# Kernel tuning notes

Measured on AMD Instinct MI355X. Metric: run time of the kernel, lower is better.

## Reference

```python
import jax, jax.numpy as jnp
import numpy as np

B, C, H, W = 256, 200, 32, 32


def setup_inputs() -> dict:
    key = jax.random.key(0)
    x = jax.random.normal(key, (B, C, H, W), dtype=jnp.float32)
    # exact init of the torch nn.Parameter: log(3.2 / c^2) * ones(1,1)
    temperature = jnp.log(3.2 / (C * C)) * jnp.ones((1, 1), dtype=jnp.float32)
    return {"x": x, "temperature": temperature}


def reference(x, temperature):
    b, c, h, w = x.shape
    xf = x.reshape(b, c, h * w)                     # (B, c, hw)
    # Gram matrix x @ x^T  -> (B, c, c)
    G = jnp.einsum('bcm,bdm->bcd', xf, xf)
    # diagonal of G = squared norms per band  -> (B, c)
    d = jnp.einsum('bcm,bcm->bc', xf, xf)
    # I_M @ (G*I) puts d_j in every row; (G*I) @ I_M puts d_i in every column
    dcov = d[:, None, :] + d[:, :, None] - 2.0 * G  # (B, c, c)
    dcov = jnp.maximum(dcov, 0.0)
    dcov = jnp.sqrt(jnp.exp(temperature)[0, 0] * dcov + 1e-5)
    # double centering: dcov@I_M/c = row means, I_M@dcov/c = col means,
    # I_M@dcov@I_M/c^2 = global mean (per batch element)
    row_mean = jnp.mean(dcov, axis=2, keepdims=True)
    col_mean = jnp.mean(dcov, axis=1, keepdims=True)
    tot_mean = jnp.mean(dcov, axis=(1, 2), keepdims=True)
    return -(dcov - row_mean - col_mean + tot_mean)
```

## Files before the change

### kernel.cpp

```cpp
#include <hip/hip_runtime.h>
#include <hip/hip_bf16.h>

typedef __bf16 bf16x8 __attribute__((ext_vector_type(8)));
typedef float  f32x4  __attribute__((ext_vector_type(4)));

#define C_DIM   200
#define HW_DIM  1024
#define NT      13
#define PADC    208
#define BK      64
#define NKC     16
#define ROWB    128
#define TILEB   (PADC*ROWB)
#define SLAB    (PADC*HW_DIM)

#define GLD16(gp, lp) __builtin_amdgcn_global_load_lds(                      \
    (const __attribute__((address_space(1))) unsigned int*)(gp),             \
    (__attribute__((address_space(3))) unsigned int*)(lp), 16, 0, 0)

__device__ __forceinline__ bf16x8 pack8(float4 a, float4 b){
  bf16x8 v;
  v[0]=(__bf16)a.x; v[1]=(__bf16)a.y; v[2]=(__bf16)a.z; v[3]=(__bf16)a.w;
  v[4]=(__bf16)b.x; v[5]=(__bf16)b.y; v[6]=(__bf16)b.z; v[7]=(__bf16)b.w;
  return v;
}

__global__ __launch_bounds__(832, 4)
void spectral_corr_kernel(const float* __restrict__ x,
                          const float* __restrict__ temp,
                          float* __restrict__ out,
                          __hip_bfloat16* __restrict__ ws)
{
  __shared__ __align__(16) char sA[2][TILEB];
  __shared__ float d_lds[PADC];
  __shared__ float rs_lds[PADC];

  const int tid = threadIdx.x;
  const int b   = blockIdx.x;
  const int w   = tid >> 6;
  const int l   = tid & 63;
  const int g   = l >> 4;
  const int c   = l & 15;

  const float*    xb = x  + (size_t)b * (C_DIM * HW_DIM);
  __hip_bfloat16* wb = ws + (size_t)b * SLAB;

  const int r_a  = tid >> 3,        c8_a = tid & 7;
  const int s_b  = tid + 832;
  const int r_b  = s_b >> 3,        c8_b = s_b & 7;
  const bool vb  = (s_b < 1600);

  const int si = l >> 3;
  const int sc = (l & 7) ^ si;
  const int i0 = 2*w, i1 = 2*w + 1;
  const __hip_bfloat16* gs0 = wb + (size_t)(8*i0 + si)*HW_DIM + sc*8;
  const __hip_bfloat16* gs1 = wb + (size_t)(8*i1 + si)*HW_DIM + sc*8;

  f32x4 acc[NT];
  #pragma unroll
  for (int j=0;j<NT;++j) acc[j] = (f32x4){0.f,0.f,0.f,0.f};

  #pragma unroll
  for (int cc = 0; cc < 2; ++cc){
    {
      const float* p = xb + (size_t)r_a*HW_DIM + cc*BK + c8_a*8;
      float4 f0 = *(const float4*)p, f1 = *(const float4*)(p+4);
      *reinterpret_cast<bf16x8*>(wb + (size_t)r_a*HW_DIM + cc*BK + c8_a*8) = pack8(f0,f1);
    }
    if (vb){
      const float* p = xb + (size_t)r_b*HW_DIM + cc*BK + c8_b*8;
      float4 f0 = *(const float4*)p, f1 = *(const float4*)(p+4);
      *reinterpret_cast<bf16x8*>(wb + (size_t)r_b*HW_DIM + cc*BK + c8_b*8) = pack8(f0,f1);
    }
  }
  __syncthreads();

  GLD16(gs0, &sA[0][i0*1024]);
  GLD16(gs1, &sA[0][i1*1024]);
  __syncthreads();

  const float et = expf(temp[0]);

  const int swz = (c & 7) << 4;
  const int rb0 = c*ROWB + ((     g*16) ^ swz);
  const int rb1 = c*ROWB + ((64 + g*16) ^ swz);

  for (int kc = 0; kc < NKC; ++kc){
    const char* bufc = sA[kc & 1];
    if (kc+1 < NKC){
      char* bufn = sA[(kc+1)&1];
      GLD16(gs0 + (kc+1)*BK, &bufn[i0*1024]);
      GLD16(gs1 + (kc+1)*BK, &bufn[i1*1024]);
    }
    float4 fa0, fa1, fb0, fb1;
    const bool cv = (kc+2 < NKC);
    if (cv){
      const float* pa = xb + (size_t)r_a*HW_DIM + (kc+2)*BK + c8_a*8;
      fa0 = *(const float4*)pa; fa1 = *(const float4*)(pa+4);
      if (vb){
        const float* pb = xb + (size_t)r_b*HW_DIM + (kc+2)*BK + c8_b*8;
        fb0 = *(const float4*)pb; fb1 = *(const float4*)(pb+4);
      }
    }
    #pragma unroll
    for (int s = 0; s < 2; ++s){
      const char* p = bufc + (s ? rb1 : rb0);
      bf16x8 fw = *reinterpret_cast<const bf16x8*>(p + w*2048);
      #pragma unroll
      for (int j = 0; j < NT; ++j){
        bf16x8 fj = *reinterpret_cast<const bf16x8*>(p + j*2048);
        acc[j] = __builtin_amdgcn_mfma_f32_16x16x32_bf16(fw, fj, acc[j], 0, 0, 0);
      }
    }
    if (cv){
      *reinterpret_cast<bf16x8*>(wb + (size_t)r_a*HW_DIM + (kc+2)*BK + c8_a*8) = pack8(fa0,fa1);
      if (vb)
        *reinterpret_cast<bf16x8*>(wb + (size_t)r_b*HW_DIM + (kc+2)*BK + c8_b*8) = pack8(fb0,fb1);
    }
    __syncthreads();
  }

  #pragma unroll
  for (int j=0;j<NT;++j){
    if (j == w){
      #pragma unroll
      for (int i=0;i<4;++i)
        if (c == g*4 + i) d_lds[j*16 + c] = acc[j][i];
    }
  }
  __syncthreads();

  float dr[4];
  #pragma unroll
  for (int i=0;i<4;++i) dr[i] = d_lds[w*16 + g*4 + i];
  float rsum[4] = {0.f,0.f,0.f,0.f};
  #pragma unroll
  for (int j=0;j<NT;++j){
    const float dc = d_lds[j*16 + c];
    const bool cvv = (j*16 + c) < C_DIM;
    #pragma unroll
    for (int i=0;i<4;++i){
      float v = dr[i] + dc - 2.0f*acc[j][i];
      v = fmaxf(v, 0.0f);
      v = sqrtf(fmaf(et, v, 1e-5f));
      acc[j][i] = v;
      if (cvv) rsum[i] += v;
    }
  }
  #pragma unroll
  for (int m=1;m<16;m<<=1){
    #pragma unroll
    for (int i=0;i<4;++i) rsum[i] += __shfl_xor(rsum[i], m, 64);
  }
  if (c == 0){
    #pragma unroll
    for (int i=0;i<4;++i) rs_lds[w*16 + g*4 + i] = rsum[i];
  }
  __syncthreads();

  float tot = 0.f;
  for (int r=0;r<C_DIM;++r) tot += rs_lds[r];
  const float inv  = 1.0f/(float)C_DIM;
  const float totm = tot*inv*inv;

  float* ob = out + b*(C_DIM*C_DIM);
  float rmr[4];
  #pragma unroll
  for (int i=0;i<4;++i) rmr[i] = rs_lds[w*16 + g*4 + i]*inv;
  #pragma unroll
  for (int j=0;j<NT;++j){
    const int col = j*16 + c;
    if (col < C_DIM){
      const float rmc = rs_lds[col]*inv;
      #pragma unroll
      for (int i=0;i<4;++i){
        const int row = w*16 + g*4 + i;
        if (row < C_DIM)
          ob[row*C_DIM + col] = rmr[i] + rmc - totm - acc[j][i];
      }
    }
  }
}

extern "C" void kernel_launch(void* const* d_in, const int* in_sizes, int n_in,
                              void* d_out, int out_size, void* d_ws, size_t ws_size,
                              hipStream_t stream) {
  const float* x    = (const float*)d_in[0];
  const float* temp = (const float*)d_in[1];
  float* out        = (float*)d_out;
  __hip_bfloat16* ws = (__hip_bfloat16*)d_ws;
  spectral_corr_kernel<<<dim3(256), dim3(832), 0, stream>>>(x, temp, out, ws);
}
```

Baseline: 341.6 us.

## Split Gram K-reduction across two blocks per batch with a finish kernel

Result: slower. 369.0 us (+8.0%).

```diff
diff --git a/kernel.cpp b/kernel.cpp
--- a/kernel.cpp
+++ b/kernel.cpp
@@ -9,10 +9,12 @@
 #define NT      13
 #define PADC    208
 #define BK      64
-#define NKC     16
+#define KHALF   8
 #define ROWB    128
 #define TILEB   (PADC*ROWB)
 #define SLAB    (PADC*HW_DIM)
+#define GSIZE   (PADC*PADC)
+#define PART_OFF ((size_t)112*1024*1024)
 
 #define GLD16(gp, lp) __builtin_amdgcn_global_load_lds(                      \
     (const __attribute__((address_space(1))) unsigned int*)(gp),             \
@@ -26,17 +28,16 @@
 }
 
 __global__ __launch_bounds__(832, 4)
-void spectral_corr_kernel(const float* __restrict__ x,
-                          const float* __restrict__ temp,
-                          float* __restrict__ out,
-                          __hip_bfloat16* __restrict__ ws)
+void gram_partial_kernel(const float* __restrict__ x,
+                         __hip_bfloat16* __restrict__ ws,
+                         float* __restrict__ part)
 {
   __shared__ __align__(16) char sA[2][TILEB];
-  __shared__ float d_lds[PADC];
-  __shared__ float rs_lds[PADC];
 
   const int tid = threadIdx.x;
-  const int b   = blockIdx.x;
+  const int b   = blockIdx.x >> 1;
+  const int h   = blockIdx.x & 1;
+  const int k0  = h * KHALF;
   const int w   = tid >> 6;
   const int l   = tid & 63;
   const int g   = l >> 4;
@@ -45,10 +46,10 @@
   const float*    xb = x  + (size_t)b * (C_DIM * HW_DIM);
   __hip_bfloat16* wb = ws + (size_t)b * SLAB;
 
-  const int r_a  = tid >> 3,        c8_a = tid & 7;
-  const int s_b  = tid + 832;
-  const int r_b  = s_b >> 3,        c8_b = s_b & 7;
-  const bool vb  = (s_b < 1600);
+  const int r_a = tid >> 3,  c8_a = tid & 7;
+  const int s_b = tid + 832;
+  const int r_b = s_b >> 3,  c8_b = s_b & 7;
+  const bool vb = (s_b < 1600);
 
   const int si = l >> 3;
   const int sc = (l & 7) ^ si;
@@ -63,43 +64,41 @@
   #pragma unroll
   for (int cc = 0; cc < 2; ++cc){
     {
-      const float* p = xb + (size_t)r_a*HW_DIM + cc*BK + c8_a*8;
-      float4 f0 = *(const float4*)p, f1 = *(const float4*)(p+4);
-      *reinterpret_cast<bf16x8*>(wb + (size_t)r_a*HW_DIM + cc*BK + c8_a*8) = pack8(f0,f1);
+      const size_t o = (size_t)r_a*HW_DIM + (k0+cc)*BK + c8_a*8;
+      float4 f0 = *(const float4*)(xb + o), f1 = *(const float4*)(xb + o + 4);
+      *reinterpret_cast<bf16x8*>(wb + o) = pack8(f0,f1);
     }
     if (vb){
-      const float* p = xb + (size_t)r_b*HW_DIM + cc*BK + c8_b*8;
-      float4 f0 = *(const float4*)p, f1 = *(const float4*)(p+4);
-      *reinterpret_cast<bf16x8*>(wb + (size_t)r_b*HW_DIM + cc*BK + c8_b*8) = pack8(f0,f1);
-    }
-  }
-  __syncthreads();
-
-  GLD16(gs0, &sA[0][i0*1024]);
-  GLD16(gs1, &sA[0][i1*1024]);
-  __syncthreads();
-
-  const float et = expf(temp[0]);
+      const size_t o = (size_t)r_b*HW_DIM + (k0+cc)*BK + c8_b*8;
+      float4 f0 = *(const float4*)(xb + o), f1 = *(const float4*)(xb + o + 4);
+      *reinterpret_cast<bf16x8*>(wb + o) = pack8(f0,f1);
+    }
+  }
+  __syncthreads();
+
+  GLD16(gs0 + k0*BK, &sA[0][i0*1024]);
+  GLD16(gs1 + k0*BK, &sA[0][i1*1024]);
+  __syncthreads();
 
   const int swz = (c & 7) << 4;
   const int rb0 = c*ROWB + ((     g*16) ^ swz);
   const int rb1 = c*ROWB + ((64 + g*16) ^ swz);
 
-  for (int kc = 0; kc < NKC; ++kc){
+  for (int kc = 0; kc < KHALF; ++kc){
     const char* bufc = sA[kc & 1];
-    if (kc+1 < NKC){
+    if (kc+1 < KHALF){
       char* bufn = sA[(kc+1)&1];
-      GLD16(gs0 + (kc+1)*BK, &bufn[i0*1024]);
-      GLD16(gs1 + (kc+1)*BK, &bufn[i1*1024]);
+      GLD16(gs0 + (k0+kc+1)*BK, &bufn[i0*1024]);
+      GLD16(gs1 + (k0+kc+1)*BK, &bufn[i1*1024]);
     }
     float4 fa0, fa1, fb0, fb1;
-    const bool cv = (kc+2 < NKC);
+    const bool cv = (kc+2 < KHALF);
     if (cv){
-      const float* pa = xb + (size_t)r_a*HW_DIM + (kc+2)*BK + c8_a*8;
-      fa0 = *(const float4*)pa; fa1 = *(const float4*)(pa+4);
+      const size_t oa = (size_t)r_a*HW_DIM + (k0+kc+2)*BK + c8_a*8;
+      fa0 = *(const float4*)(xb + oa); fa1 = *(const float4*)(xb + oa + 4);
       if (vb){
-        const float* pb = xb + (size_t)r_b*HW_DIM + (kc+2)*BK + c8_b*8;
-        fb0 = *(const float4*)pb; fb1 = *(const float4*)(pb+4);
+        const size_t ob = (size_t)r_b*HW_DIM + (k0+kc+2)*BK + c8_b*8;
+        fb0 = *(const float4*)(xb + ob); fb1 = *(const float4*)(xb + ob + 4);
       }
     }
     #pragma unroll
@@ -113,11 +112,54 @@
       }
     }
     if (cv){
-      *reinterpret_cast<bf16x8*>(wb + (size_t)r_a*HW_DIM + (kc+2)*BK + c8_a*8) = pack8(fa0,fa1);
-      if (vb)
-        *reinterpret_cast<bf16x8*>(wb + (size_t)r_b*HW_DIM + (kc+2)*BK + c8_b*8) = pack8(fb0,fb1);
+      const size_t oa = (size_t)r_a*HW_DIM + (k0+kc+2)*BK + c8_a*8;
+      *reinterpret_cast<bf16x8*>(wb + oa) = pack8(fa0,fa1);
+      if (vb){
+        const size_t ob = (size_t)r_b*HW_DIM + (k0+kc+2)*BK + c8_b*8;
+        *reinterpret_cast<bf16x8*>(wb + ob) = pack8(fb0,fb1);
+      }
     }
     __syncthreads();
+  }
+
+  float* pb = part + (size_t)(2*b + h) * GSIZE;
+  #pragma unroll
+  for (int j=0;j<NT;++j){
+    #pragma unroll
+    for (int i=0;i<4;++i){
+      const int row = w*16 + g*4 + i;
+      pb[row*PADC + j*16 + c] = acc[j][i];
+    }
+  }
+}
+
+__global__ __launch_bounds__(832, 4)
+void dcov_finish_kernel(const float* __restrict__ part,
+                        const float* __restrict__ temp,
+                        float* __restrict__ out)
+{
+  __shared__ float d_lds[PADC];
+  __shared__ float rs_lds[PADC];
+
+  const int tid = threadIdx.x;
+  const int b   = blockIdx.x;
+  const int w   = tid >> 6;
+  const int l   = tid & 63;
+  const int g   = l >> 4;
+  const int c   = l & 15;
+
+  const float* p0 = part + (size_t)(2*b    ) * GSIZE;
+  const float* p1 = part + (size_t)(2*b + 1) * GSIZE;
+  const float et  = expf(temp[0]);
+
+  f32x4 acc[NT];
+  #pragma unroll
+  for (int j=0;j<NT;++j){
+    #pragma unroll
+    for (int i=0;i<4;++i){
+      const int idx = (w*16 + g*4 + i)*PADC + j*16 + c;
+      acc[j][i] = p0[idx] + p1[idx];
+    }
   }
 
   #pragma unroll
@@ -189,5 +231,7 @@
   const float* temp = (const float*)d_in[1];
   float* out        = (float*)d_out;
   __hip_bfloat16* ws = (__hip_bfloat16*)d_ws;
-  spectral_corr_kernel<<<dim3(256), dim3(832), 0, stream>>>(x, temp, out, ws);
-}
+  float* part       = (float*)((char*)d_ws + PART_OFF);
+  gram_partial_kernel<<<dim3(512), dim3(832), 0, stream>>>(x, ws, part);
+  dcov_finish_kernel <<<dim3(256), dim3(832), 0, stream>>>(part, temp, out);
+}
```
